# Optimization experiments

Measured on AMD Instinct MI355X. Metric: run time of the kernel, lower is better.

Reference implementation:

```python
import jax, jax.numpy as jnp
import numpy as np

NUM_CLASSES = 80
LAMBDA_OBJ, LAMBDA_NOOBJ, LAMBDA_BBOX, LAMBDA_CLASS = 1.0, 0.5, 5.0, 1.0
IOU_POS = 0.5
ALPHA, GAMMA = 0.25, 2.0


def setup_inputs() -> dict:
    key = jax.random.key(0)
    ks = jax.random.split(key, 7)
    B, A, H, W, C, M = 8, 3, 80, 80, NUM_CLASSES, 100
    objectness = jax.random.uniform(ks[0], (B, A, H, W, 1), dtype=jnp.float32)
    xy = jax.random.uniform(ks[1], (B, A, H, W, 2), dtype=jnp.float32)
    wh = 0.05 + 0.25 * jax.random.uniform(ks[2], (B, A, H, W, 2), dtype=jnp.float32)
    boxes = jnp.concatenate([xy, wh], axis=-1)  # (cx,cy,w,h)
    class_scores = jax.random.normal(ks[3], (B, A, H, W, C), dtype=jnp.float32)
    txy = jax.random.uniform(ks[4], (B, M, 2), dtype=jnp.float32)
    twh = 0.05 + 0.25 * jax.random.uniform(ks[5], (B, M, 2), dtype=jnp.float32)
    target_boxes = jnp.concatenate([txy, twh], axis=-1)
    target_labels = jax.random.randint(ks[6], (B, M), 0, C)
    return {"objectness": objectness, "boxes": boxes, "class_scores": class_scores,
            "target_boxes": target_boxes, "target_labels": target_labels}


def _box_iou(b1, b2):
    # b1: [N,4], b2: [M,4] in (cx,cy,w,h) -> IoU [N,M]
    b1_lo = b1[:, :2] - b1[:, 2:] * 0.5
    b1_hi = b1[:, :2] + b1[:, 2:] * 0.5
    b2_lo = b2[:, :2] - b2[:, 2:] * 0.5
    b2_hi = b2[:, :2] + b2[:, 2:] * 0.5
    lo = jnp.maximum(b1_lo[:, None, :], b2_lo[None, :, :])
    hi = jnp.minimum(b1_hi[:, None, :], b2_hi[None, :, :])
    wh = jnp.clip(hi - lo, 0.0)
    inter = wh[..., 0] * wh[..., 1]
    a1 = b1[:, 2] * b1[:, 3]
    a2 = b2[:, 2] * b2[:, 3]
    union = a1[:, None] + a2[None, :] - inter
    return inter / (union + 1e-6)


def _giou(b1, b2):
    # elementwise pairs [N,4],[N,4] -> [N]
    b1_lo = b1[:, :2] - b1[:, 2:] * 0.5
    b1_hi = b1[:, :2] + b1[:, 2:] * 0.5
    b2_lo = b2[:, :2] - b2[:, 2:] * 0.5
    b2_hi = b2[:, :2] + b2[:, 2:] * 0.5
    wh = jnp.clip(jnp.minimum(b1_hi, b2_hi) - jnp.maximum(b1_lo, b2_lo), 0.0)
    inter = wh[:, 0] * wh[:, 1]
    union = b1[:, 2] * b1[:, 3] + b2[:, 2] * b2[:, 3] - inter
    iou = inter / (union + 1e-6)
    ewh = jnp.clip(jnp.maximum(b1_hi, b2_hi) - jnp.minimum(b1_lo, b2_lo), 0.0)
    enclose = ewh[:, 0] * ewh[:, 1]
    return iou - (enclose - union) / (enclose + 1e-6)


def _per_image(obj, boxes, cls, tb, tl):
    # obj:[N], boxes:[N,4], cls:[N,C], tb:[M,4], tl:[M]
    N = boxes.shape[0]
    iou = _box_iou(boxes, tb)                 # [N,M] -- dominant intermediate
    max_iou = jnp.max(iou, axis=1)
    idx = jnp.argmax(iou, axis=1)
    pos = max_iou >= IOU_POS
    posf = pos.astype(boxes.dtype)
    bbox_t = tb[idx] * posf[:, None]          # zeros for negatives
    class_t = jnp.where(pos, tl[idx], 0)
    # objectness BCE (torch BCELoss clamps log terms at -100), summed over anchors
    logp = jnp.maximum(jnp.log(obj), -100.0)
    log1mp = jnp.maximum(jnp.log1p(-obj), -100.0)
    bce_sum = -jnp.sum(posf * logp + (1.0 - posf) * log1mp)
    pos_cnt = jnp.sum(posf)
    # faithful to source: scalar BCE sum broadcast over masks then re-summed
    obj_term = bce_sum * (LAMBDA_OBJ * pos_cnt + LAMBDA_NOOBJ * (N - pos_cnt))
    # GIoU bbox loss over positive anchors
    giou = _giou(boxes, bbox_t)
    bbox_sum = jnp.sum((1.0 - giou) * posf)
    # focal loss (logits) vs one-hot, mean over positive subset [P,C]
    onehot = jax.nn.one_hot(class_t, NUM_CLASSES, dtype=cls.dtype)
    p = jax.nn.sigmoid(cls)
    ce = jnp.maximum(cls, 0.0) - cls * onehot + jnp.log1p(jnp.exp(-jnp.abs(cls)))
    p_t = p * onehot + (1.0 - p) * (1.0 - onehot)
    a_t = ALPHA * onehot + (1.0 - ALPHA) * (1.0 - onehot)
    fl = a_t * (1.0 - p_t) ** GAMMA * ce
    class_sum = jnp.sum(fl * posf[:, None]) / jnp.maximum(pos_cnt * NUM_CLASSES, 1.0)
    return obj_term, bbox_sum, class_sum, pos_cnt


def _forward(objectness, boxes, class_scores, target_boxes, target_labels):
    B = objectness.shape[0]
    obj_f = objectness.reshape(B, -1)
    box_f = boxes.reshape(B, -1, 4)
    cls_f = class_scores.reshape(B, -1, NUM_CLASSES)
    o, bb, cl, pc = jax.vmap(_per_image)(obj_f, box_f, cls_f, target_boxes, target_labels)
    num_pos = jnp.maximum(jnp.sum(pc), 1.0)
    obj_loss = jnp.sum(o) / B
    bbox_loss = LAMBDA_BBOX * jnp.sum(bb) / num_pos
    class_loss = LAMBDA_CLASS * jnp.sum(cl) / B
    return obj_loss + bbox_loss + class_loss


def reference(objectness, boxes, class_scores, target_boxes, target_labels):
    return _forward(objectness, boxes, class_scores, target_boxes, target_labels)
```

## Files before the change

### kernel.cpp

```cpp
#include <hip/hip_runtime.h>
#include <math.h>

#define NCLS   80
#define MTGT   100
#define NANCH  19200
#define BATCH  8
#define BLK    64
#define NBLK   (NANCH / BLK)

__device__ __forceinline__ float fast_rcp(float x) { return __builtin_amdgcn_rcpf(x); }

__device__ __forceinline__ float focal_term(float x, bool is_t) {
    const float ax  = fabsf(x);
    const float q   = __expf(-ax);
    const float ce0 = fmaxf(x, 0.0f) + __logf(1.0f + q);
    const float r   = fast_rcp(1.0f + q);
    const float p   = (x >= 0.0f) ? r : q * r;
    const float pt  = is_t ? (1.0f - p) : p;
    const float ce  = is_t ? (ce0 - x) : ce0;
    const float at  = is_t ? 0.25f : 0.75f;
    return at * pt * pt * ce;
}

__global__ __launch_bounds__(BLK) void anchor_kernel(
    const float* __restrict__ obj, const float* __restrict__ boxes,
    const float* __restrict__ cls, const float* __restrict__ tb,
    const int* __restrict__ tl, float4* __restrict__ partials)
{
    __shared__ float4 t_box[MTGT];
    __shared__ float  t_area[MTGT];
    __shared__ int    t_lab[MTGT];
    const int b    = blockIdx.y;
    const int lane = threadIdx.x;

    for (int m = lane; m < MTGT; m += BLK) {
        const float4 t = ((const float4*)tb)[b * MTGT + m];
        t_box[m]  = make_float4(t.x - 0.5f * t.z, t.y - 0.5f * t.w,
                                t.x + 0.5f * t.z, t.y + 0.5f * t.w);
        t_area[m] = t.z * t.w;
        t_lab[m]  = tl[b * MTGT + m];
    }
    __syncthreads();

    const int i   = blockIdx.x * BLK + lane;
    const int gid = b * NANCH + i;

    const float4 bx = ((const float4*)boxes)[gid];
    const float lox = bx.x - 0.5f * bx.z, loy = bx.y - 0.5f * bx.w;
    const float hix = bx.x + 0.5f * bx.z, hiy = bx.y + 0.5f * bx.w;
    const float a1  = bx.z * bx.w;
    const float aa  = a1 + 1e-6f;

    float best = -1.0f; int bidx = 0;
    #pragma unroll 10
    for (int m = 0; m < MTGT; ++m) {
        const float4 t = t_box[m];
        float iw = fmaxf(fminf(hix, t.z) - fmaxf(lox, t.x), 0.0f);
        float ih = fmaxf(fminf(hiy, t.w) - fmaxf(loy, t.y), 0.0f);
        float inter = iw * ih;
        float uni   = aa + t_area[m] - inter;
        float iou   = inter * fast_rcp(uni);
        if (iou > best) { best = iou; bidx = m; }
    }

    const bool  pos  = (best >= 0.5f);
    const float posf = pos ? 1.0f : 0.0f;

    const float o   = obj[gid];
    const float bce = -fmaxf(__logf(pos ? o : 1.0f - o), -100.0f);

    float bbox_l = 0.0f;
    float focal  = 0.0f;
    if (pos) {
        const float4 t = t_box[bidx];
        float iw = fmaxf(fminf(hix, t.z) - fmaxf(lox, t.x), 0.0f);
        float ih = fmaxf(fminf(hiy, t.w) - fmaxf(loy, t.y), 0.0f);
        float inter = iw * ih;
        float uni   = a1 + t_area[bidx] - inter;
        float iou   = inter * fast_rcp(uni + 1e-6f);
        float ew = fmaxf(fmaxf(hix, t.z) - fminf(lox, t.x), 0.0f);
        float eh = fmaxf(fmaxf(hiy, t.w) - fminf(loy, t.y), 0.0f);
        float enc  = ew * eh;
        float giou = iou - (enc - uni) * fast_rcp(enc + 1e-6f);
        bbox_l = 1.0f - giou;

        const int c = t_lab[bidx];
        const float4* row = (const float4*)(cls + (long)gid * NCLS);
        #pragma unroll
        for (int j4 = 0; j4 < NCLS / 4; ++j4) {
            const float4 v = row[j4];
            focal += focal_term(v.x, 4 * j4 + 0 == c);
            focal += focal_term(v.y, 4 * j4 + 1 == c);
            focal += focal_term(v.z, 4 * j4 + 2 == c);
            focal += focal_term(v.w, 4 * j4 + 3 == c);
        }
    }

    float v0 = bce, v1 = posf, v2 = bbox_l, v3 = focal;
    #pragma unroll
    for (int off = 32; off; off >>= 1) {
        v0 += __shfl_down(v0, off);
        v1 += __shfl_down(v1, off);
        v2 += __shfl_down(v2, off);
        v3 += __shfl_down(v3, off);
    }
    if (lane == 0)
        partials[b * NBLK + blockIdx.x] = make_float4(v0, v1, v2, v3);
}

__global__ __launch_bounds__(512) void finalize_kernel(
    const float4* __restrict__ partials, float* __restrict__ out)
{
    const int wave = threadIdx.x >> 6;
    const int lane = threadIdx.x & 63;

    float s0 = 0.f, s1 = 0.f, s2 = 0.f, s3 = 0.f;
    for (int blk = lane; blk < NBLK; blk += 64) {
        const float4 p = partials[wave * NBLK + blk];
        s0 += p.x; s1 += p.y; s2 += p.z; s3 += p.w;
    }
    #pragma unroll
    for (int off = 32; off; off >>= 1) {
        s0 += __shfl_down(s0, off);
        s1 += __shfl_down(s1, off);
        s2 += __shfl_down(s2, off);
        s3 += __shfl_down(s3, off);
    }
    __shared__ float img[BATCH][4];
    if (lane == 0) { img[wave][0] = s0; img[wave][1] = s1; img[wave][2] = s2; img[wave][3] = s3; }
    __syncthreads();
    if (threadIdx.x == 0) {
        float sum_pc = 0.f, obj_l = 0.f, bbox_s = 0.f, cls_l = 0.f;
        #pragma unroll
        for (int b = 0; b < BATCH; ++b) {
            const float bce = img[b][0];
            const float pc  = img[b][1];
            const float bb  = img[b][2];
            const float fo  = img[b][3];
            sum_pc += pc;
            obj_l  += bce * (1.0f * pc + 0.5f * ((float)NANCH - pc));
            bbox_s += bb;
            cls_l  += fo / fmaxf(pc * (float)NCLS, 1.0f);
        }
        const float num_pos = fmaxf(sum_pc, 1.0f);
        out[0] = obj_l / (float)BATCH + 5.0f * bbox_s / num_pos + cls_l / (float)BATCH;
    }
}

extern "C" void kernel_launch(void* const* d_in, const int* in_sizes, int n_in,
                              void* d_out, int out_size, void* d_ws, size_t ws_size,
                              hipStream_t stream) {
    const float* obj   = (const float*)d_in[0];
    const float* boxes = (const float*)d_in[1];
    const float* cls   = (const float*)d_in[2];
    const float* tb    = (const float*)d_in[3];
    const int*   tl    = (const int*)d_in[4];
    float* out = (float*)d_out;

    float4* partials = (float4*)d_ws;

    dim3 gridA(NBLK, BATCH);
    anchor_kernel<<<gridA, BLK, 0, stream>>>(obj, boxes, cls, tb, tl, partials);
    finalize_kernel<<<1, 512, 0, stream>>>(partials, out);
}
```

Measured before the change: 119.7 us.

## Split IoU target scan across four waves and compare IoU without division

```diff
diff --git a/kernel.cpp b/kernel.cpp
--- a/kernel.cpp
+++ b/kernel.cpp
@@ -1,12 +1,14 @@
 #include <hip/hip_runtime.h>
 #include <math.h>
 
-#define NCLS   80
-#define MTGT   100
-#define NANCH  19200
-#define BATCH  8
-#define BLK    64
-#define NBLK   (NANCH / BLK)
+#define NCLS    80
+#define MTGT    100
+#define NANCH   19200
+#define BATCH   8
+#define BLKA    64
+#define NBLK    (NANCH / BLKA)
+#define NWAVE   4
+#define TSLICE  (MTGT / NWAVE)
 
 __device__ __forceinline__ float fast_rcp(float x) { return __builtin_amdgcn_rcpf(x); }
 
@@ -22,7 +24,7 @@
     return at * pt * pt * ce;
 }
 
-__global__ __launch_bounds__(BLK) void anchor_kernel(
+__global__ __launch_bounds__(256) void anchor_kernel(
     const float* __restrict__ obj, const float* __restrict__ boxes,
     const float* __restrict__ cls, const float* __restrict__ tb,
     const int* __restrict__ tl, float4* __restrict__ partials)
@@ -30,20 +32,26 @@
     __shared__ float4 t_box[MTGT];
     __shared__ float  t_area[MTGT];
     __shared__ int    t_lab[MTGT];
+    __shared__ float  m_bi[NWAVE][BLKA];
+    __shared__ float  m_bu[NWAVE][BLKA];
+    __shared__ int    m_ix[NWAVE][BLKA];
+
     const int b    = blockIdx.y;
-    const int lane = threadIdx.x;
+    const int tid  = threadIdx.x;
+    const int wave = tid >> 6;
+    const int lane = tid & 63;
 
-    for (int m = lane; m < MTGT; m += BLK) {
-        const float4 t = ((const float4*)tb)[b * MTGT + m];
-        t_box[m]  = make_float4(t.x - 0.5f * t.z, t.y - 0.5f * t.w,
-                                t.x + 0.5f * t.z, t.y + 0.5f * t.w);
-        t_area[m] = t.z * t.w;
-        t_lab[m]  = tl[b * MTGT + m];
+    if (tid < MTGT) {
+        const float4 t = ((const float4*)tb)[b * MTGT + tid];
+        t_box[tid]  = make_float4(t.x - 0.5f * t.z, t.y - 0.5f * t.w,
+                                  t.x + 0.5f * t.z, t.y + 0.5f * t.w);
+        t_area[tid] = t.z * t.w;
+        t_lab[tid]  = tl[b * MTGT + tid];
     }
     __syncthreads();
 
-    const int i   = blockIdx.x * BLK + lane;
-    const int gid = b * NANCH + i;
+    const int a   = blockIdx.x * BLKA + lane;
+    const int gid = b * NANCH + a;
 
     const float4 bx = ((const float4*)boxes)[gid];
     const float lox = bx.x - 0.5f * bx.z, loy = bx.y - 0.5f * bx.w;
@@ -51,19 +59,33 @@
     const float a1  = bx.z * bx.w;
     const float aa  = a1 + 1e-6f;
 
-    float best = -1.0f; int bidx = 0;
-    #pragma unroll 10
-    for (int m = 0; m < MTGT; ++m) {
+    float bi = -1.0f, bu = 1.0f; int bidx = 0;
+    const int m0 = wave * TSLICE;
+    #pragma unroll
+    for (int mm = 0; mm < TSLICE; ++mm) {
+        const int m = m0 + mm;
         const float4 t = t_box[m];
         float iw = fmaxf(fminf(hix, t.z) - fmaxf(lox, t.x), 0.0f);
         float ih = fmaxf(fminf(hiy, t.w) - fmaxf(loy, t.y), 0.0f);
         float inter = iw * ih;
         float uni   = aa + t_area[m] - inter;
-        float iou   = inter * fast_rcp(uni);
-        if (iou > best) { best = iou; bidx = m; }
+        if (inter * bu > bi * uni) { bi = inter; bu = uni; bidx = m; }
+    }
+    m_bi[wave][lane] = bi;
+    m_bu[wave][lane] = bu;
+    m_ix[wave][lane] = bidx;
+    __syncthreads();
+
+    if (wave != 0) return;
+
+    float Bi = m_bi[0][lane], Bu = m_bu[0][lane]; int Bx = m_ix[0][lane];
+    #pragma unroll
+    for (int w = 1; w < NWAVE; ++w) {
+        const float ci = m_bi[w][lane], cu = m_bu[w][lane];
+        if (ci * Bu > Bi * cu) { Bi = ci; Bu = cu; Bx = m_ix[w][lane]; }
     }
 
-    const bool  pos  = (best >= 0.5f);
+    const bool  pos  = (Bi + Bi >= Bu);
     const float posf = pos ? 1.0f : 0.0f;
 
     const float o   = obj[gid];
@@ -72,19 +94,16 @@
     float bbox_l = 0.0f;
     float focal  = 0.0f;
     if (pos) {
-        const float4 t = t_box[bidx];
-        float iw = fmaxf(fminf(hix, t.z) - fmaxf(lox, t.x), 0.0f);
-        float ih = fmaxf(fminf(hiy, t.w) - fmaxf(loy, t.y), 0.0f);
-        float inter = iw * ih;
-        float uni   = a1 + t_area[bidx] - inter;
-        float iou   = inter * fast_rcp(uni + 1e-6f);
-        float ew = fmaxf(fmaxf(hix, t.z) - fminf(lox, t.x), 0.0f);
-        float eh = fmaxf(fmaxf(hiy, t.w) - fminf(loy, t.y), 0.0f);
-        float enc  = ew * eh;
-        float giou = iou - (enc - uni) * fast_rcp(enc + 1e-6f);
+        const float4 t   = t_box[Bx];
+        const float uni  = a1 + t_area[Bx] - Bi;
+        const float iou  = Bi * fast_rcp(Bu);
+        const float ew   = fmaxf(fmaxf(hix, t.z) - fminf(lox, t.x), 0.0f);
+        const float eh   = fmaxf(fmaxf(hiy, t.w) - fminf(loy, t.y), 0.0f);
+        const float enc  = ew * eh;
+        const float giou = iou - (enc - uni) * fast_rcp(enc + 1e-6f);
         bbox_l = 1.0f - giou;
 
-        const int c = t_lab[bidx];
+        const int c = t_lab[Bx];
         const float4* row = (const float4*)(cls + (long)gid * NCLS);
         #pragma unroll
         for (int j4 = 0; j4 < NCLS / 4; ++j4) {
@@ -160,6 +179,6 @@
     float4* partials = (float4*)d_ws;
 
     dim3 gridA(NBLK, BATCH);
-    anchor_kernel<<<gridA, BLK, 0, stream>>>(obj, boxes, cls, tb, tl, partials);
+    anchor_kernel<<<gridA, 256, 0, stream>>>(obj, boxes, cls, tb, tl, partials);
     finalize_kernel<<<1, 512, 0, stream>>>(partials, out);
 }
```

New measurement: 115.1 us. 3.8% less time.
